# Optimization experiments

Hardware: AMD Instinct MI355X
Metric: run time of the kernel (lower is better)

The kernel has to match this reference:

```python
import jax, jax.numpy as jnp
import numpy as np

N_NODES = 50000
N_EDGES = 800000
MUL = 16            # multiplicity of each irrep (16x0e + 16x1o)
RADIAL_IN = 8       # radial basis size
RADIAL_HID = 64
N_PATHS = 5         # TP paths: s*Y0->s, v.Yv->s, s*Yv->v, v*Y0->v, v x Yv->v
NUM_SPECIES = 4
AVG_NEIGH = 16.0


def setup_inputs() -> dict:
    key = jax.random.key(0)
    ks = jax.random.split(key, 16)
    inp = {
        'node_scalars': jax.random.normal(ks[0], (N_NODES, MUL), jnp.float32),
        'node_vectors': jax.random.normal(ks[1], (N_NODES, MUL * 3), jnp.float32),
        'edge_sh': jax.random.normal(ks[2], (N_EDGES, 4), jnp.float32),
        'radial_emb': jax.random.uniform(ks[3], (N_EDGES, RADIAL_IN), jnp.float32),
        'senders': jax.random.randint(ks[4], (N_EDGES,), 0, N_NODES, jnp.int32),
        'receivers': jax.random.randint(ks[5], (N_EDGES,), 0, N_NODES, jnp.int32),
        'species': jax.random.randint(ks[6], (N_NODES,), 0, NUM_SPECIES, jnp.int32),
        # learned params (fan-in scaled)
        'W_in_s': jax.random.normal(ks[7], (MUL, MUL), jnp.float32) / np.sqrt(MUL),
        'W_in_v': jax.random.normal(ks[8], (MUL, MUL), jnp.float32) / np.sqrt(MUL),
        'mlp_w1': jax.random.normal(ks[9], (RADIAL_IN, RADIAL_HID), jnp.float32) / np.sqrt(RADIAL_IN),
        'mlp_b1': jnp.zeros((RADIAL_HID,), jnp.float32),
        'mlp_w2': jax.random.normal(ks[10], (RADIAL_HID, N_PATHS * MUL), jnp.float32) / np.sqrt(RADIAL_HID),
        'W_out_s': jax.random.normal(ks[11], (2 * MUL, 2 * MUL), jnp.float32) / np.sqrt(2 * MUL),
        'W_out_v': jax.random.normal(ks[12], (3 * MUL, MUL), jnp.float32) / np.sqrt(3 * MUL),
        'sc_s': jax.random.normal(ks[13], (NUM_SPECIES, MUL, 2 * MUL), jnp.float32) / np.sqrt(MUL),
        'sc_v': jax.random.normal(ks[14], (NUM_SPECIES, MUL, MUL), jnp.float32) / np.sqrt(MUL),
    }
    return inp


def reference(node_scalars, node_vectors, edge_sh, radial_emb, senders, receivers,
              species, W_in_s, W_in_v, mlp_w1, mlp_b1, mlp_w2, W_out_s, W_out_v,
              sc_s, sc_v):
    N = node_scalars.shape[0]
    inv_sqrt_deg = 1.0 / np.sqrt(AVG_NEIGH)

    # ---- input per-irrep linear ----
    s = node_scalars @ W_in_s                                  # [N,16]
    v_in = node_vectors.reshape(N, MUL, 3)
    v = jnp.einsum('nuc,uw->nwc', v_in, W_in_v)                # [N,16,3]

    # ---- gather sender features ----
    xs = s[senders]                                            # [E,16]
    xv = v[senders]                                            # [E,16,3]
    Y0 = edge_sh[:, :1]                                        # [E,1] l=0 SH
    Yv = edge_sh[:, 1:4]                                       # [E,3] l=1 SH

    # ---- radial MLP -> per-path tensor-product weights ----
    h = jax.nn.silu(radial_emb @ mlp_w1 + mlp_b1)              # [E,64]
    w = (h @ mlp_w2).reshape(-1, N_PATHS, MUL)                 # [E,5,16]

    # ---- CG tensor product (uvu) messages ----
    m_s1 = w[:, 0] * xs * Y0                                   # 0e x 0e -> 0e
    m_s2 = w[:, 1] * jnp.einsum('euc,ec->eu', xv, Yv)          # 1o x 1o -> 0e (dot)
    m_v1 = w[:, 2, :, None] * xs[:, :, None] * Yv[:, None, :]  # 0e x 1o -> 1o
    m_v2 = w[:, 3, :, None] * xv * Y0[:, :, None]              # 1o x 0e -> 1o
    m_v3 = w[:, 4, :, None] * jnp.cross(xv, Yv[:, None, :])    # 1o x 1o -> 1o (cross)

    # ---- scatter-sum to receivers + neighbour normalization ----
    m_s = jnp.concatenate([m_s1, m_s2], axis=-1)               # [E,32]
    m_v = jnp.concatenate([m_v1, m_v2, m_v3], axis=1)          # [E,48,3]
    a_s = jax.ops.segment_sum(m_s, receivers, num_segments=N) * inv_sqrt_deg
    a_v = jax.ops.segment_sum(m_v, receivers, num_segments=N) * inv_sqrt_deg

    # ---- output per-irrep linear ----
    pre_s = a_s @ W_out_s                                      # [N,32]
    pre_v = jnp.einsum('nuc,uw->nwc', a_v, W_out_v)            # [N,16,3]

    # ---- species-dependent self connection ----
    pre_s = pre_s + jnp.einsum('nu,nuw->nw', node_scalars, sc_s[species])
    pre_v = pre_v + jnp.einsum('nuc,nuw->nwc', v_in, sc_v[species])

    # ---- gate nonlinearity ----
    out_s = jax.nn.silu(pre_s[:, :MUL])                        # scalar outputs
    gates = jax.nn.sigmoid(pre_s[:, MUL:])                     # gate scalars
    out_v = pre_v * gates[:, :, None]

    # ---- resnet ----
    out_s = out_s + node_scalars
    out_v = out_v + v_in

    return jnp.concatenate([out_s, out_v.reshape(N, MUL * 3)], axis=-1)
```

## Files before the change

### kernel.cpp

```cpp
#include <hip/hip_runtime.h>
#include <hip/hip_bf16.h>

typedef unsigned short u16;
typedef unsigned int   u32;
typedef _Float16 h2 __attribute__((ext_vector_type(2)));
typedef short s8v __attribute__((ext_vector_type(8)));
typedef float f4v __attribute__((ext_vector_type(4)));
typedef u16 u16x4 __attribute__((ext_vector_type(4)));

#define N_NODES 50000
#define N_EDGES 800000
#define NCH   2
#define RPC   25000
#define CHMAX 409600

#define RPB   250
#define NBINS 200
#define EPB   4096
#define NBB   ((N_EDGES+EPB-1)/EPB)

#define WB_W1H  0
#define WB_B1   256
#define WB_W2F  320
#define WB_WINS 2880
#define WB_WINV 3136
#define WB_WOS  3392
#define WB_WOV  4416
#define WB_SCS  5184
#define WB_SCV  7232
#define WB_FLAG 8256
#define OFF_SV16 8260
#define IDX_BCNT 1608260
#define IDX_BOF2 1608516
#define IDX_BCUR 1608772
#define IDX_OFFS 1658260
#define IDX_BUCK 1758262
#define IDX_EEID 2558264
#define OFF_ER16 3358264
#define OFF_WP   3758264
#define ACC_OFF  29972664

__device__ __forceinline__ float bf2f(u16 v){
  union { u32 u; float f; } x; x.u = ((u32)v) << 16; return x.f;
}
__device__ __forceinline__ u16 f2bf(float f){
  u32 u = __float_as_uint(f);
  u32 lsb = (u >> 16) & 1u;
  u32 r = u + 0x7fffu + lsb;
  return (u16)(r >> 16);
}
__device__ __forceinline__ float ldx(const void* p, long long i, int isf){
  return isf ? ((const float*)p)[i] : bf2f(((const u16*)p)[i]);
}
__device__ __forceinline__ u32 pkh2(float a, float b){
  union { u32 u; h2 v; } x; x.v.x = (_Float16)a; x.v.y = (_Float16)b; return x.u;
}
__device__ __forceinline__ float dot2(h2 a, u32 w, float c){
  union { u32 u; h2 v; } x; x.u = w;
#if __has_builtin(__builtin_amdgcn_fdot2)
  return __builtin_amdgcn_fdot2(a, x.v, c, false);
#else
  return c + (float)a.x*(float)x.v.x + (float)a.y*(float)x.v.y;
#endif
}
__device__ __forceinline__ float sigmoidf_(float x){ return 1.f/(1.f + __expf(-x)); }

__global__ void detect_dtype(const u32* __restrict__ remb_raw, int* __restrict__ flag){
  int t = threadIdx.x;
  u32 w = remb_raw[t];
  u32 lo = w & 0xffffu, hi = w >> 16;
  int okl = ((lo & 0x8000u) == 0) && (((lo >> 7) & 0xffu) <= 126u);
  int okh = ((hi & 0x8000u) == 0) && (((hi >> 7) & 0xffu) <= 126u);
  unsigned long long bad = __ballot(!(okl && okh));
  if (t == 0) *flag = (bad != 0ull) ? 1 : 0;
}

__global__ void prep_weights(const void* __restrict__ w1, const void* __restrict__ b1g,
                             const void* __restrict__ w2, const void* __restrict__ wins,
                             const void* __restrict__ winv, const void* __restrict__ wos,
                             const void* __restrict__ wov, const void* __restrict__ scs,
                             const void* __restrict__ scv, float* __restrict__ wbuf,
                             const int* __restrict__ flag){
  int t = threadIdx.x;
  int isf = *flag;
  u32* w1h  = (u32*)(wbuf + WB_W1H);
  u16* w2f  = (u16*)(wbuf + WB_W2F);
  for (int idx=t; idx<256;  idx+=256){
    int j = idx>>2, ip = idx&3;
    w1h[idx] = pkh2(ldx(w1, (2*ip)*64+j, isf), ldx(w1, (2*ip+1)*64+j, isf));
  }
  for (int idx=t; idx<64;   idx+=256){ wbuf[WB_B1+idx]  = ldx(b1g, idx, isf); }
  for (int idx=t; idx<5120; idx+=256){
    int tt = idx >> 10;
    int rem = idx & 1023;
    int kh = rem >> 9;
    int rem2 = rem & 511;
    int ln = rem2 >> 3, j = rem2 & 7;
    int k = kh*32 + (ln>>4)*8 + j;
    int o = tt*16 + (ln&15);
    w2f[idx] = f2bf(ldx(w2, (long long)k*80 + o, isf));
  }
  for (int idx=t; idx<256;  idx+=256){ wbuf[WB_WINS+idx] = ldx(wins, idx, isf); }
  for (int idx=t; idx<256;  idx+=256){ wbuf[WB_WINV+idx] = ldx(winv, idx, isf); }
  for (int idx=t; idx<1024; idx+=256){ wbuf[WB_WOS+idx]  = ldx(wos, idx, isf); }
  for (int idx=t; idx<768;  idx+=256){ wbuf[WB_WOV+idx]  = ldx(wov, idx, isf); }
  for (int idx=t; idx<2048; idx+=256){ wbuf[WB_SCS+idx]  = ldx(scs, idx, isf); }
  for (int idx=t; idx<1024; idx+=256){ wbuf[WB_SCV+idx]  = ldx(scv, idx, isf); }
}

__global__ void __launch_bounds__(64) node_pre(
    const void* __restrict__ ns_g, const void* __restrict__ nv_g,
    const float* __restrict__ wbuf, u16* __restrict__ sv16,
    const int* __restrict__ flag){
  int n = blockIdx.x*64 + threadIdx.x;
  if (n >= N_NODES) return;
  int isf = *flag;
  float a[16], b[48];
  if (isf){
    const f4v* pa = (const f4v*)ns_g + (size_t)n*4;
    #pragma unroll
    for (int k=0;k<4;k++){
      f4v v = pa[k];
      a[k*4]=v[0]; a[k*4+1]=v[1]; a[k*4+2]=v[2]; a[k*4+3]=v[3];
    }
    const f4v* pb = (const f4v*)nv_g + (size_t)n*12;
    #pragma unroll
    for (int k=0;k<12;k++){
      f4v v = pb[k];
      b[k*4]=v[0]; b[k*4+1]=v[1]; b[k*4+2]=v[2]; b[k*4+3]=v[3];
    }
  } else {
    const s8v* pa = (const s8v*)ns_g + (size_t)n*2;
    #pragma unroll
    for (int k=0;k<2;k++){
      s8v v = pa[k];
      #pragma unroll
      for (int j=0;j<8;j++) a[k*8+j] = bf2f((u16)v[j]);
    }
    const s8v* pb = (const s8v*)nv_g + (size_t)n*6;
    #pragma unroll
    for (int k=0;k<6;k++){
      s8v v = pb[k];
      #pragma unroll
      for (int j=0;j<8;j++) b[k*8+j] = bf2f((u16)v[j]);
    }
  }
  const float* wins = wbuf + WB_WINS;
  const float* winv = wbuf + WB_WINV;
  float s[16];
  #pragma unroll
  for (int w=0;w<16;w++) s[w]=0.f;
  #pragma unroll
  for (int u=0;u<16;u++){
    float au = a[u];
    #pragma unroll
    for (int w=0;w<16;w++) s[w] += au * wins[u*16+w];
  }
  float v0[16], v1[16], v2[16];
  #pragma unroll
  for (int w=0;w<16;w++){ v0[w]=0.f; v1[w]=0.f; v2[w]=0.f; }
  #pragma unroll
  for (int u=0;u<16;u++){
    float bu0=b[u*3], bu1=b[u*3+1], bu2=b[u*3+2];
    #pragma unroll
    for (int w=0;w<16;w++){
      float wv = winv[u*16+w];
      v0[w] += bu0*wv; v1[w] += bu1*wv; v2[w] += bu2*wv;
    }
  }
  s8v* svp = (s8v*)(sv16 + (size_t)n*64);
  #pragma unroll
  for (int w=0;w<16;w+=2){
    s8v pk;
    pk[0]=(short)f2bf(s[w]);   pk[1]=(short)f2bf(v0[w]);
    pk[2]=(short)f2bf(v1[w]);  pk[3]=(short)f2bf(v2[w]);
    pk[4]=(short)f2bf(s[w+1]); pk[5]=(short)f2bf(v0[w+1]);
    pk[6]=(short)f2bf(v1[w+1]);pk[7]=(short)f2bf(v2[w+1]);
    svp[w>>1] = pk;
  }
}

__global__ void __launch_bounds__(256) bin_count(const int* __restrict__ receivers,
                                                 int* __restrict__ bcnt){
  __shared__ int lcnt[NBINS];
  int t = threadIdx.x;
  for (int i=t;i<NBINS;i+=256) lcnt[i]=0;
  __syncthreads();
  int base = blockIdx.x*EPB;
  for (int i=t;i<EPB;i+=256){
    int e = base+i;
    if (e<N_EDGES) atomicAdd(&lcnt[receivers[e]/RPB],1);
  }
  __syncthreads();
  for (int i=t;i<NBINS;i+=256) if (lcnt[i]) atomicAdd(&bcnt[i], lcnt[i]);
}

__global__ void bin_scan(const int* __restrict__ bcnt, int* __restrict__ binoff,
                         int* __restrict__ bincur, int* __restrict__ offs){
  __shared__ int lds[NBINS];
  int t=threadIdx.x;
  if (t<NBINS) lds[t]=bcnt[t];
  __syncthreads();
  for (int off=1; off<NBINS; off<<=1){
    int v = (t<NBINS && t>=off)? lds[t-off] : 0;
    __syncthreads();
    if (t<NBINS) lds[t]+=v;
    __syncthreads();
  }
  if (t<NBINS){ int ex = lds[t]-bcnt[t]; binoff[t]=ex; bincur[t]=ex; }
  if (t==0) offs[N_NODES] = N_EDGES;
}

__global__ void __launch_bounds__(256) bin_scatter(const int* __restrict__ receivers,
                 int* __restrict__ bincur, u32* __restrict__ eeid, u16* __restrict__ er){
  __shared__ int lcnt[NBINS], loff[NBINS], lcur[NBINS], gbase[NBINS];
  __shared__ u32 seid[EPB];
  __shared__ u16 sr[EPB];
  int t = threadIdx.x;
  for (int i=t;i<NBINS;i+=256) lcnt[i]=0;
  __syncthreads();
  int base = blockIdx.x*EPB;
  int r_[16];
  #pragma unroll
  for (int k=0;k<16;k++){
    int e = base + t + k*256;
    r_[k] = (e<N_EDGES)? receivers[e] : -1;
    if (r_[k]>=0) atomicAdd(&lcnt[r_[k]/RPB],1);
  }
  __syncthreads();
  if (t<NBINS) loff[t]=lcnt[t];
  __syncthreads();
  for (int off=1; off<NBINS; off<<=1){
    int v=(t<NBINS&&t>=off)?loff[t-off]:0;
    __syncthreads();
    if (t<NBINS) loff[t]+=v;
    __syncthreads();
  }
  if (t<NBINS){
    int ex=loff[t]-lcnt[t]; loff[t]=ex; lcur[t]=ex;
    gbase[t] = lcnt[t] ? atomicAdd(&bincur[t], lcnt[t]) : 0;
  }
  __syncthreads();
  #pragma unroll
  for (int k=0;k<16;k++){
    if (r_[k]>=0){
      int b=r_[k]/RPB;
      int p=atomicAdd(&lcur[b],1);
      seid[p]=(u32)(base + t + k*256);
      sr[p]=(u16)r_[k];
    }
  }
  __syncthreads();
  int rem = N_EDGES - base;
  int tot = rem < EPB ? rem : EPB;
  for (int i=t;i<tot;i+=256){
    int b = sr[i]/RPB;
    int dst = gbase[b] + (i - loff[b]);
    eeid[dst]=seid[i]; er[dst]=sr[i];
  }
}

__global__ void __launch_bounds__(256) bin_finalize(const u32* __restrict__ eeid,
        const u16* __restrict__ er, const int* __restrict__ binoff,
        const int* __restrict__ bcnt, int* __restrict__ offs, int* __restrict__ bucket){
  __shared__ int deg[RPB], pfx[RPB], lcur[RPB];
  int b=blockIdx.x, t=threadIdx.x;
  int beg=binoff[b], cnt=bcnt[b];
  for (int i=t;i<RPB;i+=256) deg[i]=0;
  __syncthreads();
  int r0=b*RPB;
  for (int i=t;i<cnt;i+=256) atomicAdd(&deg[er[beg+i]-r0],1);
  __syncthreads();
  if (t<RPB) pfx[t]=deg[t];
  __syncthreads();
  for (int off=1; off<RPB; off<<=1){
    int v=(t<RPB&&t>=off)?pfx[t-off]:0;
    __syncthreads();
    if (t<RPB) pfx[t]+=v;
    __syncthreads();
  }
  if (t<RPB){
    int ex=pfx[t]-deg[t]; pfx[t]=ex; lcur[t]=ex;
    offs[r0+t]=beg+ex;
  }
  __syncthreads();
  for (int i=t;i<cnt;i+=256){
    int rr = er[beg+i]-r0;
    int k = atomicAdd(&lcur[rr],1);
    bucket[beg+k] = (int)eeid[beg+i];
  }
}

__global__ void __launch_bounds__(256) pass1_w(
    const int* __restrict__ bucket, const int* __restrict__ offs,
    const void* __restrict__ remb, const float* __restrict__ wbuf,
    u16* __restrict__ wp16, int rlo, const int* __restrict__ flag){
  __shared__ u16 hlds[4*16*72];
  int tid = threadIdx.x;
  int lane = tid & 63, wid = tid >> 6;
  int isf = *flag;
  int chunkBeg = offs[rlo], chunkEnd = offs[rlo + RPC];
  int r0e = chunkBeg + (blockIdx.x*4 + wid)*16;
  if (r0e >= chunkEnd) return;
  u16* hw = hlds + wid*(16*72);
  int e = lane & 15, q = lane >> 4;

  int er = r0e + e;
  int eid = (er < chunkEnd) ? bucket[er] : 0;
  float re[8];
  if (isf){
    f4v ra = ((const f4v*)remb)[(size_t)eid*2];
    f4v rb = ((const f4v*)remb)[(size_t)eid*2+1];
    re[0]=ra[0]; re[1]=ra[1]; re[2]=ra[2]; re[3]=ra[3];
    re[4]=rb[0]; re[5]=rb[1]; re[6]=rb[2]; re[7]=rb[3];
  } else {
    s8v r8 = ((const s8v*)remb)[eid];
    #pragma unroll
    for (int i=0;i<8;i++) re[i] = bf2f((u16)r8[i]);
  }
  h2 reh[4];
  #pragma unroll
  for (int ip=0;ip<4;ip++){ reh[ip].x=(_Float16)re[2*ip]; reh[ip].y=(_Float16)re[2*ip+1]; }
  const u32* w1h = (const u32*)(wbuf + WB_W1H);
  const float* b1 = wbuf + WB_B1;
  #pragma unroll
  for (int jj=0;jj<16;jj++){
    int j = q*16 + jj;
    float a = b1[j];
    #pragma unroll
    for (int ip=0;ip<4;ip++) a = dot2(reh[ip], w1h[j*4+ip], a);
    a = a * sigmoidf_(a);
    hw[e*72 + j] = f2bf(a);
  }
  asm volatile("s_waitcnt lgkmcnt(0)" ::: "memory");

  const u16* w2f = (const u16*)(wbuf + WB_W2F);
  s8v bfr[5][2];
  #pragma unroll
  for (int t=0;t<5;t++)
    #pragma unroll
    for (int kh=0;kh<2;kh++)
      bfr[t][kh] = *(const s8v*)(w2f + ((t*2+kh)*64 + lane)*8);

  f4v acc[5];
  #pragma unroll
  for (int t=0;t<5;t++) acc[t] = (f4v){0.f,0.f,0.f,0.f};
  #pragma unroll
  for (int kh=0;kh<2;kh++){
    s8v af = *(const s8v*)(hw + e*72 + kh*32 + q*8);
    #pragma unroll
    for (int t=0;t<5;t++)
      acc[t] = __builtin_amdgcn_mfma_f32_16x16x32_bf16(af, bfr[t][kh], acc[t], 0,0,0);
  }
  int n = lane & 15;
  #pragma unroll
  for (int r=0;r<4;r++){
    int er2 = r0e + q*4 + r;
    if (er2 < chunkEnd){
      size_t widx = (size_t)(er2 - chunkBeg);
      s8v pk;
      pk[0]=(short)f2bf(acc[0][r]); pk[1]=(short)f2bf(acc[1][r]);
      pk[2]=(short)f2bf(acc[2][r]); pk[3]=(short)f2bf(acc[3][r]);
      pk[4]=(short)f2bf(acc[4][r]); pk[5]=0; pk[6]=0; pk[7]=0;
      *(s8v*)(wp16 + (widx*16 + n)*8) = pk;
    }
  }
}

__global__ void __launch_bounds__(256, 4) pass2_reduce(
    const int* __restrict__ bucket, const int* __restrict__ offs,
    const void* __restrict__ edge_sh, const int* __restrict__ senders,
    const u16* __restrict__ sv16, const u16* __restrict__ wp16,
    float* __restrict__ accbuf, int rlo, const int* __restrict__ flag){
  __shared__ float part[4][176];
  int tid = threadIdx.x;
  int lane = tid & 63, wid = tid >> 6;
  int u = lane & 15, q = lane >> 4;
  int pr = wid >> 1;
  int wsub = wid & 1;
  int isf = *flag;
  int r = rlo + blockIdx.x*2 + pr;
  int chunkBeg = offs[rlo];
  int beg = offs[r], end = offs[r+1];
  float As0=0.f,As1=0.f;
  float Av00=0.f,Av01=0.f,Av02=0.f, Av10=0.f,Av11=0.f,Av12=0.f, Av20=0.f,Av21=0.f,Av22=0.f;
  auto body = [&](int rank){
    int eid = bucket[rank];
    float Y0,Yv0,Yv1,Yv2;
    if (isf){
      f4v y = ((const f4v*)edge_sh)[eid];
      Y0=y[0]; Yv0=y[1]; Yv1=y[2]; Yv2=y[3];
    } else {
      u16x4 y = ((const u16x4*)edge_sh)[eid];
      Y0=bf2f(y[0]); Yv0=bf2f(y[1]); Yv1=bf2f(y[2]); Yv2=bf2f(y[3]);
    }
    int snd = senders[eid];
    s8v wv = *(const s8v*)(wp16 + ((size_t)(rank - chunkBeg)*16 + u)*8);
    float w0=bf2f((u16)wv[0]), w1=bf2f((u16)wv[1]), w2=bf2f((u16)wv[2]);
    float w3=bf2f((u16)wv[3]), w4=bf2f((u16)wv[4]);
    u16x4 sv = *(const u16x4*)(sv16 + ((size_t)snd*16 + u)*4);
    float xs=bf2f(sv[0]), x0=bf2f(sv[1]), x1=bf2f(sv[2]), x2=bf2f(sv[3]);
    As0 += w0*xs*Y0;
    As1 += w1*(x0*Yv0 + x1*Yv1 + x2*Yv2);
    float t1 = w2*xs;  Av00 += t1*Yv0; Av01 += t1*Yv1; Av02 += t1*Yv2;
    float t2 = w3*Y0;  Av10 += t2*x0;  Av11 += t2*x1;  Av12 += t2*x2;
    Av20 += w4*(x1*Yv2 - x2*Yv1);
    Av21 += w4*(x2*Yv0 - x0*Yv2);
    Av22 += w4*(x0*Yv1 - x1*Yv0);
  };
  int rank = beg + wsub*4 + q;
  for (; rank + 8 < end; rank += 16){ body(rank); body(rank+8); }
  if (rank < end) body(rank);
  #define RED2(x) { x += __shfl_xor(x,16); x += __shfl_xor(x,32); }
  RED2(As0) RED2(As1)
  RED2(Av00) RED2(Av01) RED2(Av02)
  RED2(Av10) RED2(Av11) RED2(Av12)
  RED2(Av20) RED2(Av21) RED2(Av22)
  #undef RED2
  if (q == 0){
    float* pp = part[wid];
    pp[u]=As0;      pp[16+u]=As1;
    pp[32+u]=Av00;  pp[48+u]=Av10;  pp[64+u]=Av20;
    pp[80+u]=Av01;  pp[96+u]=Av11;  pp[112+u]=Av21;
    pp[128+u]=Av02; pp[144+u]=Av12; pp[160+u]=Av22;
  }
  __syncthreads();
  for (int i = tid; i < 352; i += 256){
    int pr2 = i / 176, idx = i - pr2*176;
    int rr = blockIdx.x*2 + pr2;
    accbuf[(size_t)rr*176 + idx] = part[pr2*2][idx] + part[pr2*2+1][idx];
  }
}

__global__ void __launch_bounds__(256) pass2_epilogue(
    const float* __restrict__ accbuf, const float* __restrict__ wbuf,
    const void* __restrict__ ns_g, const void* __restrict__ nv_g,
    const int* __restrict__ species, void* __restrict__ out,
    int rlo, const int* __restrict__ flag){
  __shared__ float sb[16*176 + 16*16 + 16*48];
  int tid = threadIdx.x;
  int isf = *flag;
  int n0 = rlo + blockIdx.x*16;
  int rem = rlo + RPC - n0;
  int nblk = rem < 16 ? rem : 16;
  {
    int tot = nblk*176;
    const float* src = accbuf + (size_t)(n0 - rlo)*176;
    for (int i=tid; i<tot; i+=256) sb[i] = src[i];
    float* nsb = sb + 2816;
    for (int i=tid; i<nblk*16; i+=256)
      nsb[i] = ldx(ns_g, (long long)n0*16 + i, isf);
    float* vinb = sb + 2816 + 256;
    for (int i=tid; i<nblk*48; i+=256)
      vinb[i] = ldx(nv_g, (long long)n0*48 + i, isf);
  }
  __syncthreads();
  int g = tid >> 4, u = tid & 15;
  if (g >= nblk) return;
  int nn = n0 + g;
  const float* bin  = sb + g*176;
  const float* nsb  = sb + 2816 + g*16;
  const float* vinb = sb + 2816 + 256 + g*48;
  int sp = species[nn];
  const float* wos = wbuf + WB_WOS;
  const float* scs = wbuf + WB_SCS + sp*512;
  const float* wov = wbuf + WB_WOV;
  const float* scv = wbuf + WB_SCV + sp*256;
  float p0 = 0.f, p1 = 0.f;
  #pragma unroll
  for (int j=0;j<32;j++){
    float a = bin[j]*0.25f;
    p0 += a*wos[j*32+u];
    p1 += a*wos[j*32+16+u];
  }
  #pragma unroll
  for (int j=0;j<16;j++){
    float nu = nsb[j];
    p0 += nu*scs[j*32+u];
    p1 += nu*scs[j*32+16+u];
  }
  float gate = sigmoidf_(p1);
  float os = p0*sigmoidf_(p0) + nsb[u];
  float pv0, pv1, pv2;
  {
    float a0=0.f, a1=0.f, a2=0.f;
    #pragma unroll
    for (int j=0;j<48;j++){
      float wv = wov[j*16+u];
      a0 += bin[32 + 0*48 + j]*0.25f*wv;
      a1 += bin[32 + 1*48 + j]*0.25f*wv;
      a2 += bin[32 + 2*48 + j]*0.25f*wv;
    }
    #pragma unroll
    for (int j=0;j<16;j++){
      float sv = scv[j*16+u];
      a0 += vinb[j*3+0]*sv;
      a1 += vinb[j*3+1]*sv;
      a2 += vinb[j*3+2]*sv;
    }
    pv0 = a0*gate + vinb[u*3+0];
    pv1 = a1*gate + vinb[u*3+1];
    pv2 = a2*gate + vinb[u*3+2];
  }
  if (isf){
    float* orow = (float*)out + (size_t)nn*64;
    orow[u] = os;
    orow[16 + u*3 + 0] = pv0;
    orow[16 + u*3 + 1] = pv1;
    orow[16 + u*3 + 2] = pv2;
  } else {
    u16* orow = (u16*)out + (size_t)nn*64;
    orow[u] = f2bf(os);
    orow[16 + u*3 + 0] = f2bf(pv0);
    orow[16 + u*3 + 1] = f2bf(pv1);
    orow[16 + u*3 + 2] = f2bf(pv2);
  }
}

extern "C" void kernel_launch(void* const* d_in, const int* in_sizes, int n_in,
                              void* d_out, int out_size, void* d_ws, size_t ws_size,
                              hipStream_t stream){
  const void* node_scalars = d_in[0];
  const void* node_vectors = d_in[1];
  const void* edge_sh      = d_in[2];
  const void* radial_emb   = d_in[3];
  const int* senders      = (const int*)d_in[4];
  const int* receivers    = (const int*)d_in[5];
  const int* species      = (const int*)d_in[6];
  const void* W_in_s  = d_in[7];
  const void* W_in_v  = d_in[8];
  const void* mlp_w1  = d_in[9];
  const void* mlp_b1  = d_in[10];
  const void* mlp_w2  = d_in[11];
  const void* W_out_s = d_in[12];
  const void* W_out_v = d_in[13];
  const void* sc_s    = d_in[14];
  const void* sc_v    = d_in[15];

  float* wsf  = (float*)d_ws;
  int*   wsi  = (int*)d_ws;
  u32*   wsu  = (u32*)d_ws;
  float* wbuf = wsf;
  u16*   sv16 = (u16*)(wsu + OFF_SV16);
  int*   bcnt = wsi + IDX_BCNT;
  int*   bof2 = wsi + IDX_BOF2;
  int*   bcur = wsi + IDX_BCUR;
  int*   offs = wsi + IDX_OFFS;
  int*   buck = wsi + IDX_BUCK;
  u32*   eeid = wsu + IDX_EEID;
  u16*   er16 = (u16*)(wsu + OFF_ER16);
  u16*   wp16 = (u16*)(wsu + OFF_WP);
  float* accb = wsf + ACC_OFF;
  int*   flag = (int*)(wbuf + WB_FLAG);

  detect_dtype<<<1,64,0,stream>>>((const u32*)radial_emb, flag);
  hipMemsetAsync(bcnt, 0, NBINS*sizeof(int), stream);
  prep_weights<<<1,256,0,stream>>>(mlp_w1, mlp_b1, mlp_w2, W_in_s, W_in_v,
                                   W_out_s, W_out_v, sc_s, sc_v, wbuf, flag);
  node_pre<<<(N_NODES+63)/64,64,0,stream>>>(node_scalars, node_vectors, wbuf,
                                            sv16, flag);
  bin_count<<<NBB,256,0,stream>>>(receivers, bcnt);
  bin_scan<<<1,256,0,stream>>>(bcnt, bof2, bcur, offs);
  bin_scatter<<<NBB,256,0,stream>>>(receivers, bcur, eeid, er16);
  bin_finalize<<<NBINS,256,0,stream>>>(eeid, er16, bof2, bcnt, offs, buck);
  for (int c = 0; c < NCH; c++){
    int rlo = c * RPC;
    pass1_w<<<CHMAX/64, 256, 0, stream>>>(buck, offs, radial_emb, wbuf, wp16, rlo, flag);
    pass2_reduce<<<RPC/2, 256, 0, stream>>>(buck, offs, edge_sh, senders,
                                            sv16, wp16, accb, rlo, flag);
    pass2_epilogue<<<(RPC+15)/16, 256, 0, stream>>>(accb, wbuf, node_scalars,
                                                    node_vectors, species,
                                                    d_out, rlo, flag);
  }
}
```

Measured before the change: 414.0 us.

## Pre-gather edge SH and senders in sorted order and compact per-edge weight storage

pass1_w now also gathers edge_sh (as float4) and senders (as u16) for each edge into arrays laid out in receiver-sorted order. It stores the five per-channel path weights as a packed 4×bf16 array plus a separate bf16 array, replacing the padded 8×bf16 record. pass2_reduce then reads these arrays contiguously instead of chasing bucket indices into edge_sh and senders, and it reads fewer bytes of weights per edge. The cost is extra writes in pass1 and storing sender ids in 16 bits, which depends on the node count staying below 65536.

```diff
diff --git a/kernel.cpp b/kernel.cpp
--- a/kernel.cpp
+++ b/kernel.cpp
@@ -37,8 +37,11 @@
 #define IDX_BUCK 1758262
 #define IDX_EEID 2558264
 #define OFF_ER16 3358264
-#define OFF_WP   3758264
-#define ACC_OFF  29972664
+#define OFF_WPA  3758264
+#define OFF_WPB  16865464
+#define OFF_YB   20142264
+#define OFF_SND  21780664
+#define ACC_OFF  21985464
 
 __device__ __forceinline__ float bf2f(u16 v){
   union { u32 u; float f; } x; x.u = ((u32)v) << 16; return x.f;
@@ -293,8 +296,11 @@
 
 __global__ void __launch_bounds__(256) pass1_w(
     const int* __restrict__ bucket, const int* __restrict__ offs,
-    const void* __restrict__ remb, const float* __restrict__ wbuf,
-    u16* __restrict__ wp16, int rlo, const int* __restrict__ flag){
+    const void* __restrict__ remb, const void* __restrict__ edge_sh,
+    const int* __restrict__ senders, const float* __restrict__ wbuf,
+    u16* __restrict__ wpA, u16* __restrict__ wpB,
+    float* __restrict__ ybf, u16* __restrict__ snd16,
+    int rlo, const int* __restrict__ flag){
   __shared__ u16 hlds[4*16*72];
   int tid = threadIdx.x;
   int lane = tid & 63, wid = tid >> 6;
@@ -307,6 +313,18 @@
 
   int er = r0e + e;
   int eid = (er < chunkEnd) ? bucket[er] : 0;
+  if (q == 0 && er < chunkEnd){
+    size_t widx = (size_t)(er - chunkBeg);
+    snd16[widx] = (u16)senders[eid];
+    f4v y;
+    if (isf){
+      y = ((const f4v*)edge_sh)[eid];
+    } else {
+      u16x4 yb = ((const u16x4*)edge_sh)[eid];
+      y[0]=bf2f(yb[0]); y[1]=bf2f(yb[1]); y[2]=bf2f(yb[2]); y[3]=bf2f(yb[3]);
+    }
+    ((f4v*)ybf)[widx] = y;
+  }
   float re[8];
   if (isf){
     f4v ra = ((const f4v*)remb)[(size_t)eid*2];
@@ -358,46 +376,40 @@
     int er2 = r0e + q*4 + r;
     if (er2 < chunkEnd){
       size_t widx = (size_t)(er2 - chunkBeg);
-      s8v pk;
-      pk[0]=(short)f2bf(acc[0][r]); pk[1]=(short)f2bf(acc[1][r]);
-      pk[2]=(short)f2bf(acc[2][r]); pk[3]=(short)f2bf(acc[3][r]);
-      pk[4]=(short)f2bf(acc[4][r]); pk[5]=0; pk[6]=0; pk[7]=0;
-      *(s8v*)(wp16 + (widx*16 + n)*8) = pk;
+      u16x4 pk4;
+      pk4[0]=f2bf(acc[0][r]); pk4[1]=f2bf(acc[1][r]);
+      pk4[2]=f2bf(acc[2][r]); pk4[3]=f2bf(acc[3][r]);
+      ((u16x4*)wpA)[widx*16 + n] = pk4;
+      wpB[widx*16 + n] = f2bf(acc[4][r]);
     }
   }
 }
 
 __global__ void __launch_bounds__(256, 4) pass2_reduce(
-    const int* __restrict__ bucket, const int* __restrict__ offs,
-    const void* __restrict__ edge_sh, const int* __restrict__ senders,
-    const u16* __restrict__ sv16, const u16* __restrict__ wp16,
-    float* __restrict__ accbuf, int rlo, const int* __restrict__ flag){
+    const int* __restrict__ offs,
+    const u16* __restrict__ sv16, const u16* __restrict__ wpA,
+    const u16* __restrict__ wpB, const float* __restrict__ ybf,
+    const u16* __restrict__ snd16, float* __restrict__ accbuf,
+    int rlo){
   __shared__ float part[4][176];
   int tid = threadIdx.x;
   int lane = tid & 63, wid = tid >> 6;
   int u = lane & 15, q = lane >> 4;
   int pr = wid >> 1;
   int wsub = wid & 1;
-  int isf = *flag;
   int r = rlo + blockIdx.x*2 + pr;
   int chunkBeg = offs[rlo];
   int beg = offs[r], end = offs[r+1];
   float As0=0.f,As1=0.f;
   float Av00=0.f,Av01=0.f,Av02=0.f, Av10=0.f,Av11=0.f,Av12=0.f, Av20=0.f,Av21=0.f,Av22=0.f;
   auto body = [&](int rank){
-    int eid = bucket[rank];
-    float Y0,Yv0,Yv1,Yv2;
-    if (isf){
-      f4v y = ((const f4v*)edge_sh)[eid];
-      Y0=y[0]; Yv0=y[1]; Yv1=y[2]; Yv2=y[3];
-    } else {
-      u16x4 y = ((const u16x4*)edge_sh)[eid];
-      Y0=bf2f(y[0]); Yv0=bf2f(y[1]); Yv1=bf2f(y[2]); Yv2=bf2f(y[3]);
-    }
-    int snd = senders[eid];
-    s8v wv = *(const s8v*)(wp16 + ((size_t)(rank - chunkBeg)*16 + u)*8);
-    float w0=bf2f((u16)wv[0]), w1=bf2f((u16)wv[1]), w2=bf2f((u16)wv[2]);
-    float w3=bf2f((u16)wv[3]), w4=bf2f((u16)wv[4]);
+    size_t li = (size_t)(rank - chunkBeg);
+    f4v y = ((const f4v*)ybf)[li];
+    float Y0=y[0], Yv0=y[1], Yv1=y[2], Yv2=y[3];
+    int snd = snd16[li];
+    u16x4 wv = ((const u16x4*)wpA)[li*16 + u];
+    float w0=bf2f(wv[0]), w1=bf2f(wv[1]), w2=bf2f(wv[2]), w3=bf2f(wv[3]);
+    float w4=bf2f(wpB[li*16 + u]);
     u16x4 sv = *(const u16x4*)(sv16 + ((size_t)snd*16 + u)*4);
     float xs=bf2f(sv[0]), x0=bf2f(sv[1]), x1=bf2f(sv[2]), x2=bf2f(sv[3]);
     As0 += w0*xs*Y0;
@@ -549,7 +561,10 @@
   int*   buck = wsi + IDX_BUCK;
   u32*   eeid = wsu + IDX_EEID;
   u16*   er16 = (u16*)(wsu + OFF_ER16);
-  u16*   wp16 = (u16*)(wsu + OFF_WP);
+  u16*   wpA  = (u16*)(wsu + OFF_WPA);
+  u16*   wpB  = (u16*)(wsu + OFF_WPB);
+  float* ybf  = wsf + OFF_YB;
+  u16*   snd16= (u16*)(wsu + OFF_SND);
   float* accb = wsf + ACC_OFF;
   int*   flag = (int*)(wbuf + WB_FLAG);
 
@@ -565,9 +580,10 @@
   bin_finalize<<<NBINS,256,0,stream>>>(eeid, er16, bof2, bcnt, offs, buck);
   for (int c = 0; c < NCH; c++){
     int rlo = c * RPC;
-    pass1_w<<<CHMAX/64, 256, 0, stream>>>(buck, offs, radial_emb, wbuf, wp16, rlo, flag);
-    pass2_reduce<<<RPC/2, 256, 0, stream>>>(buck, offs, edge_sh, senders,
-                                            sv16, wp16, accb, rlo, flag);
+    pass1_w<<<CHMAX/64, 256, 0, stream>>>(buck, offs, radial_emb, edge_sh, senders,
+                                          wbuf, wpA, wpB, ybf, snd16, rlo, flag);
+    pass2_reduce<<<RPC/2, 256, 0, stream>>>(offs, sv16, wpA, wpB, ybf, snd16,
+                                            accb, rlo);
     pass2_epilogue<<<(RPC+15)/16, 256, 0, stream>>>(accb, wbuf, node_scalars,
                                                     node_vectors, species,
                                                     d_out, rlo, flag);
```

New measurement: 376.2 us. -9.1%, faster.
